# Optimization experiments

Hardware: AMD Instinct MI355X
Metric: run time of the kernel (lower is better)

The kernel has to match this reference:

```python
import jax, jax.numpy as jnp
import numpy as np

DIM = 128
HEADS = 8
DK = DIM // HEADS
HID = DIM * 4
# torch: scores / math.sqrt(scale) with scale = 1/dim**0.5  ->  multiply by dim**0.25
INV = float(1.0 / np.sqrt(1.0 / np.sqrt(DIM)))


def _ln(x, g, b, eps=1e-5):
    m = jnp.mean(x, axis=-1, keepdims=True)
    v = jnp.mean((x - m) ** 2, axis=-1, keepdims=True)
    return (x - m) / jnp.sqrt(v + eps) * g + b


def _lin(x, w, b):  # torch Linear: x @ W.T + b, W:[out,in]
    return jnp.einsum('...i,oi->...o', x, w) + b


def _attention_new(node, edge, w, bv):
    # node [b,n,c], edge [b,n,n,c]; raw torch .view => row-major reshape
    b, n, c = node.shape
    q = _lin(node, w[0], bv[0]).reshape(b, HEADS, n, DK)
    k = _lin(edge, w[1], bv[1]).reshape(b, HEADS, n, n, DK)
    v = _lin(node, w[2], bv[2]).reshape(b, HEADS, n, DK)
    s = jnp.einsum('bhmd,bhmnd->bhmn', q, k) * INV
    out_attn = jax.nn.softmax(s, axis=-1)
    in_attn = jax.nn.softmax(jnp.swapaxes(s, -1, -2), axis=-1)
    eye = jnp.eye(n, dtype=s.dtype)
    # out_attn + in_attn - diag_embed(diagonal(out_attn))
    message = out_attn + in_attn - eye * out_attn
    node_h = jnp.einsum('bhmn,bhnd->bhmd', message, v).reshape(b, n, c)
    edge_h = jnp.einsum('bhmn,bhand->bhamd', message, k).reshape(b, n, n, c)
    return _lin(node_h, w[4], bv[4]), _lin(edge_h, w[3], bv[3]), message


def _enc_dec_attention(mx, px, ma, pa, w, bv):
    b, n, c = mx.shape
    P = px.shape[1]
    qx = _lin(mx, w[0], bv[0]).reshape(b, HEADS, n, DK)
    kx = _lin(px, w[1], bv[1]).reshape(b, HEADS, P, DK)
    vx = _lin(mx, w[2], bv[2]).reshape(b, HEADS, n, DK)
    qa = _lin(ma, w[3], bv[3]).reshape(b, HEADS, n, n, DK)
    ka = _lin(pa, w[4], bv[4]).reshape(b, HEADS, P, P, DK)
    va = _lin(ma, w[5], bv[5]).reshape(b, HEADS, n, n, DK)
    s = jnp.einsum('bhmd,bhnd->bhmn', qx, kx) * INV  # [b,h,n,P]
    out_attn = jax.nn.softmax(s, axis=-1)
    in_attn = jax.nn.softmax(jnp.swapaxes(s, -1, -2), axis=-1)
    message = out_attn + jnp.swapaxes(in_attn, -1, -2)
    # einsum 'bhmn,bhmd->bhmd': sum over n, elementwise scale of v
    node_h = jnp.sum(message, axis=-1)[..., None] * vx
    # 'bhmnd,bhkjd->bhmn': contract d after summing key over (k,j)
    ksum = jnp.sum(ka, axis=(2, 3))  # [b,h,d]
    se = jnp.einsum('bhmnd,bhd->bhmn', qa, ksum) * INV
    oa = jax.nn.softmax(se, axis=-1)
    ia = jax.nn.softmax(jnp.swapaxes(se, -1, -2), axis=-1)
    me = oa + jnp.swapaxes(ia, -1, -2)
    # 'bhmn,bhmkd->bhmnd': contract k
    edge_h = me[..., None] * jnp.sum(va, axis=3)[:, :, :, None, :]
    node_h = _lin(node_h.reshape(b, n, c), w[6], bv[6])
    edge_h = _lin(edge_h.reshape(b, n, n, c), w[7], bv[7])
    return edge_h, node_h, message


def _mlp(x, w1, b1, w2, b2):
    return _lin(jax.nn.sigmoid(_lin(x, w1, b1)), w2, b2)


def _decoder_block(mol_annot, prot_annot, mol_adj, prot_adj,
                   att_w, att_b, dec_w, dec_b,
                   mlp_w1, mlp_b1, mlp_w2, mlp_b2, ln_g, ln_b):
    mx = _ln(mol_annot, ln_g[2], ln_b[2])
    px = _ln(prot_annot, ln_g[3], ln_b[3])
    ma = _ln(mol_adj, ln_g[0], ln_b[0])
    pa = _ln(prot_adj, ln_g[1], ln_b[1])
    px1, pa1, _ = _attention_new(px, pa, att_w, att_b)
    px1 = _ln(px + px1, ln_g[5], ln_b[5])
    pa1 = _ln(pa + pa1, ln_g[4], ln_b[4])
    ma1, mx1, attn_dec = _enc_dec_attention(mx, px1, ma, pa1, dec_w, dec_b)
    ma1 = _ln(ma + ma1, ln_g[6], ln_b[6])
    mx1 = _ln(mx + mx1, ln_g[7], ln_b[7])
    ma2 = _mlp(ma1, mlp_w1[0], mlp_b1[0], mlp_w2[0], mlp_b2[0]) + ma1
    mx2 = _mlp(mx1, mlp_w1[1], mlp_b1[1], mlp_w2[1], mlp_b2[1]) + mx1
    edge_hidden = _ln(ma2, ln_g[8], ln_b[8])
    node_hidden = _ln(mx2, ln_g[9], ln_b[9])
    return edge_hidden, node_hidden, attn_dec


def setup_inputs() -> dict:
    key = jax.random.key(0)
    ks = jax.random.split(key, 16)
    B, N, P = 8, 64, 256
    inp = {
        'mol_annot': jax.random.normal(ks[0], (B, N, DIM), jnp.float32),
        'prot_annot': jax.random.normal(ks[1], (B, P, DIM), jnp.float32),
        'mol_adj': jax.random.normal(ks[2], (B, N, N, DIM), jnp.float32),
        'prot_adj': jax.random.normal(ks[3], (B, P, P, DIM), jnp.float32),
        # Attention_new linears: [q,k,v,out_e,out_n]
        'att_w': jax.random.normal(ks[4], (5, DIM, DIM), jnp.float32) * 0.02,
        'att_b': jax.random.normal(ks[5], (5, DIM), jnp.float32) * 0.02,
        # enc_dec linears: [q_mx,k_px,v_mx,q_ma,k_pa,v_ma,out_mx,out_ma]
        'dec_w': jax.random.normal(ks[6], (8, DIM, DIM), jnp.float32) * 0.02,
        'dec_b': jax.random.normal(ks[7], (8, DIM), jnp.float32) * 0.02,
        # MLPs: index 0 = mlp_ma, 1 = mlp_mx
        'mlp_w1': jax.random.normal(ks[8], (2, HID, DIM), jnp.float32) * 0.02,
        'mlp_b1': jax.random.normal(ks[9], (2, HID), jnp.float32) * 0.02,
        'mlp_w2': jax.random.normal(ks[10], (2, DIM, HID), jnp.float32) * 0.02,
        'mlp_b2': jax.random.normal(ks[11], (2, DIM), jnp.float32) * 0.02,
        # LayerNorms: [ln1_ma,ln1_pa,ln1_mx,ln1_px,ln2_pa,ln2_px,ln3_ma,ln3_mx,ln4_ma,ln4_mx]
        'ln_g': jnp.ones((10, DIM), jnp.float32),
        'ln_b': jnp.zeros((10, DIM), jnp.float32),
    }
    return inp


def reference(mol_annot, prot_annot, mol_adj, prot_adj, att_w, att_b,
              dec_w, dec_b, mlp_w1, mlp_b1, mlp_w2, mlp_b2, ln_g, ln_b):
    return _decoder_block(mol_annot, prot_annot, mol_adj, prot_adj,
                          att_w, att_b, dec_w, dec_b,
                          mlp_w1, mlp_b1, mlp_w2, mlp_b2, ln_g, ln_b)
```

## Files before the change

### kernel.cpp

```cpp
#include <hip/hip_runtime.h>
#include <hip/hip_bf16.h>
#include <math.h>

#define INV_SCALE 3.3635856610148585f

typedef float f32x4 __attribute__((ext_vector_type(4)));
typedef short bf16x8 __attribute__((ext_vector_type(8)));
typedef unsigned short u16;
#define MFMA(a_, b_, c_) __builtin_amdgcn_mfma_f32_16x16x32_bf16(a_, b_, c_, 0, 0, 0)

constexpr int WT_ATT = 0;
constexpr int WT_DEC = 81920;
constexpr int WT_M1  = 212992;
constexpr int WT_M2  = 344064;
constexpr int O_PX   = 475136;
constexpr int O_MX   = 737280;
constexpr int O_MA   = 802816;
constexpr int O_QL   = 4997120;
constexpr int O_VL   = 5259264;
constexpr int O_QXL  = 5521408;
constexpr int O_VXL  = 5586944;
constexpr int O_KXL  = 5652480;
constexpr int O_PX1  = 5914624;
constexpr int O_MX1  = 6176768;
constexpr int O_S    = 6242304;
constexpr int O_MSG  = 10469376;
constexpr int O_NH   = 14663680;
constexpr int O_RS   = 14925824;
constexpr int O_KS   = 14934016;
constexpr int O_SE   = 14935040;
constexpr int O_ME2  = 15197184;
constexpr int O_VAS  = 15459328;
constexpr int O_MROW = 15524864;
constexpr int O_S2   = 15528960;
constexpr int O_MA1  = 16577536;

constexpr int OUT1_OFF = 4194304;
constexpr int OUT2_OFF = 4259840;

__device__ __forceinline__ float waveSum(float v) {
#pragma unroll
  for (int o = 32; o > 0; o >>= 1) v += __shfl_down(v, o, 64);
  return v;
}

__device__ __forceinline__ void split1(float a, u16& h, u16& l) {
  unsigned ua = __float_as_uint(a) & 0xffff0000u;
  h = (u16)(ua >> 16);
  float al = a - __uint_as_float(ua);
  l = (u16)(__float_as_uint(al) >> 16);
}
__device__ __forceinline__ void split8(const float* p, bf16x8& hi, bf16x8& lo) {
#pragma unroll
  for (int i = 0; i < 8; i++) {
    float a = p[i];
    unsigned ua = __float_as_uint(a) & 0xffff0000u;
    float al = a - __uint_as_float(ua);
    hi[i] = (short)(u16)(ua >> 16);
    lo[i] = (short)(u16)(__float_as_uint(al) >> 16);
  }
}
__device__ __forceinline__ u16 rne1(float a) {
  unsigned u = __float_as_uint(a);
  u += 0x7fffu + ((u >> 16) & 1u);
  return (u16)(u >> 16);
}
__device__ __forceinline__ bf16x8 rne8(const float* p) {
  bf16x8 h;
#pragma unroll
  for (int i = 0; i < 8; i++) h[i] = (short)rne1(p[i]);
  return h;
}

__global__ __launch_bounds__(256) void prep_wt(
    const float* __restrict__ att_w, const float* __restrict__ dec_w,
    const float* __restrict__ mlp_w1, const float* __restrict__ mlp_w2,
    float* __restrict__ ws) {
  int seg = blockIdx.x, t = threadIdx.x;
  if (seg < 5) {
    const float* w = att_w + seg * 16384;
    if (seg == 1 || seg == 3) {
      u16* oh = (u16*)(ws + WT_ATT + seg * 16384);
      for (int idx = t; idx < 16384; idx += 256) {
        int e = idx & 7, lane = (idx >> 3) & 63, kk = (idx >> 9) & 3, q = idx >> 11;
        int o = q * 16 + (lane & 15), i = kk * 32 + (lane >> 4) * 8 + e;
        u16 hh, ll; split1(w[o * 128 + i], hh, ll);
        oh[idx] = hh; oh[16384 + idx] = ll;
      }
    } else {
      float* o = ws + WT_ATT + seg * 16384;
      for (int idx = t; idx < 16384; idx += 256) o[idx] = w[(idx & 127) * 128 + (idx >> 7)];
    }
  } else if (seg < 13) {
    int k = seg - 5;
    const float* w = dec_w + k * 16384;
    float* o = ws + WT_DEC + k * 16384;
    for (int idx = t; idx < 16384; idx += 256) o[idx] = w[(idx & 127) * 128 + (idx >> 7)];
  } else if (seg < 15) {
    int k = seg - 13;
    const float* w = mlp_w1 + k * 65536;
    u16* oh = (u16*)(ws + WT_M1 + k * 65536);
    for (int idx = t; idx < 65536; idx += 256) {
      int e = idx & 7, lane = (idx >> 3) & 63, kk = (idx >> 9) & 3, q = idx >> 11;
      int o = q * 16 + (lane & 15), i = kk * 32 + (lane >> 4) * 8 + e;
      oh[idx] = rne1(w[o * 128 + i]); oh[65536 + idx] = 0;
    }
  } else {
    int k = seg - 15;
    const float* w = mlp_w2 + k * 65536;
    u16* oh = (u16*)(ws + WT_M2 + k * 65536);
    for (int idx = t; idx < 65536; idx += 256) {
      int e = idx & 7, lane = (idx >> 3) & 63, kk = (idx >> 9) & 15, q = idx >> 13;
      int o = q * 16 + (lane & 15), i = kk * 32 + (lane >> 4) * 8 + e;
      oh[idx] = rne1(w[o * 512 + i]); oh[65536 + idx] = 0;
    }
  }
}

__global__ __launch_bounds__(128) void ln_rows4(const float* __restrict__ in, float* __restrict__ out,
                                                const float* __restrict__ g, const float* __restrict__ b) {
  int t = threadIdx.x;
  size_t row = (size_t)blockIdx.x * 4 + (t >> 5);
  int c4 = (t & 31) * 4;
  float4 x = *(const float4*)&in[row * 128 + c4];
  float s = x.x + x.y + x.z + x.w;
#pragma unroll
  for (int o = 16; o > 0; o >>= 1) s += __shfl_xor(s, o, 64);
  float mean = s * (1.f / 128.f);
  float dx = x.x - mean, dy = x.y - mean, dz = x.z - mean, dw = x.w - mean;
  float v = dx * dx + dy * dy + dz * dz + dw * dw;
#pragma unroll
  for (int o = 16; o > 0; o >>= 1) v += __shfl_xor(v, o, 64);
  float rstd = rsqrtf(v * (1.f / 128.f) + 1e-5f);
  float4 gv = *(const float4*)&g[c4];
  float4 bv = *(const float4*)&b[c4];
  float4 o4;
  o4.x = dx * rstd * gv.x + bv.x;
  o4.y = dy * rstd * gv.y + bv.y;
  o4.z = dz * rstd * gv.z + bv.z;
  o4.w = dw * rstd * gv.w + bv.w;
  *(float4*)&out[row * 128 + c4] = o4;
}

__global__ __launch_bounds__(128) void lin_rows2(const float* __restrict__ in,
                                                 float* __restrict__ out1, const float* __restrict__ WT1,
                                                 const float* __restrict__ b1v,
                                                 float* __restrict__ out2, const float* __restrict__ WT2,
                                                 const float* __restrict__ b2v) {
  int row = blockIdx.x, t = threadIdx.x;
  __shared__ float rl[128];
  rl[t] = in[(size_t)row * 128 + t];
  __syncthreads();
  float a1 = b1v[t], a2 = b2v[t];
#pragma unroll 8
  for (int i = 0; i < 128; i++) {
    float rv = rl[i];
    a1 += rv * WT1[i * 128 + t];
    a2 += rv * WT2[i * 128 + t];
  }
  out1[(size_t)row * 128 + t] = a1;
  out2[(size_t)row * 128 + t] = a2;
}

__global__ __launch_bounds__(128) void lin_rows(const float* __restrict__ in, float* __restrict__ out,
                                                const float* __restrict__ WT, const float* __restrict__ bias) {
  int row = blockIdx.x, t = threadIdx.x;
  __shared__ float rl[128];
  rl[t] = in[(size_t)row * 128 + t];
  __syncthreads();
  float acc = bias[t];
#pragma unroll 8
  for (int i = 0; i < 128; i++) acc += rl[i] * WT[i * 128 + t];
  out[(size_t)row * 128 + t] = acc;
}

__device__ __forceinline__ void ln32_stats(float (*tile)[132], float* psum, float* meanL, float* rstdL,
                                           int t) {
  int r = t >> 3, seg = t & 7;
  float p = 0;
#pragma unroll
  for (int k = 0; k < 16; k++) p += tile[r][seg * 16 + k];
  psum[r * 8 + seg] = p;
  __syncthreads();
  if (t < 32) { float sm = 0; for (int k = 0; k < 8; k++) sm += psum[t * 8 + k]; meanL[t] = sm * (1.f / 128.f); }
  __syncthreads();
  float mu = meanL[r];
  p = 0;
#pragma unroll
  for (int k = 0; k < 16; k++) { float d = tile[r][seg * 16 + k] - mu; p += d * d; }
  psum[r * 8 + seg] = p;
  __syncthreads();
  if (t < 32) { float sm = 0; for (int k = 0; k < 8; k++) sm += psum[t * 8 + k]; rstdL[t] = rsqrtf(sm * (1.f / 128.f) + 1e-5f); }
  __syncthreads();
}

__device__ __forceinline__ void ln128_stats(float (*tile)[132], float* psum, float* meanL, float* rstdL,
                                            int t) {
  int r = t >> 2, seg = t & 3;
  float p = 0;
#pragma unroll
  for (int k = 0; k < 32; k++) p += tile[r][seg * 32 + k];
  psum[r * 4 + seg] = p;
  __syncthreads();
  if (t < 128) meanL[t] = (psum[t * 4] + psum[t * 4 + 1] + psum[t * 4 + 2] + psum[t * 4 + 3]) * (1.f / 128.f);
  __syncthreads();
  float mu = meanL[r];
  p = 0;
#pragma unroll
  for (int k = 0; k < 32; k++) { float d = tile[r][seg * 32 + k] - mu; p += d * d; }
  psum[r * 4 + seg] = p;
  __syncthreads();
  if (t < 128) rstdL[t] = rsqrtf((psum[t * 4] + psum[t * 4 + 1] + psum[t * 4 + 2] + psum[t * 4 + 3]) * (1.f / 128.f) + 1e-5f);
  __syncthreads();
}

__global__ __launch_bounds__(256, 8) void k1_fold(
    const float* __restrict__ prot_adj, const float* __restrict__ q_lin,
    const float* __restrict__ wk_orig,
    const float* __restrict__ bk,
    const float* __restrict__ g1, const float* __restrict__ b1,
    float* __restrict__ sdst) {
  __shared__ __align__(16) float paF[32][132];
  __shared__ float wq[8][132];
  __shared__ float qL[16];
  __shared__ float psum[256];
  __shared__ float meanL[32], rstdL[32];
  int t = threadIdx.x, bid = blockIdx.x;
  int b = bid >> 11, h = (bid >> 8) & 7, ai = bid & 255;
  int irow = h * 32 + (ai >> 3), j0 = (ai & 7) * 32;
  int mq = (ai >> 3) * 8 + (ai & 7);
  size_t pabase = (((size_t)(b * 256) + irow) * 256 + j0) * 128;
  {
    const float4* src4 = (const float4*)(prot_adj + pabase);
    for (int idx = t; idx < 1024; idx += 256)
      *(float4*)&paF[idx >> 5][(idx & 31) * 4] = src4[idx];
  }
  if (t < 16) qL[t] = q_lin[((size_t)(b * 256) + h * 32 + (mq >> 3)) * 128 + (mq & 7) * 16 + t];
  __syncthreads();
#pragma unroll
  for (int k = 0; k < 4; k++) {
    int o = t + k * 256;
    int g8 = o >> 7, c = o & 127;
    float s = 0;
#pragma unroll
    for (int d = 0; d < 16; d++) s += qL[d] * wk_orig[(g8 * 16 + d) * 128 + c];
    wq[g8][c] = s;
  }
  ln32_stats(paF, psum, meanL, rstdL, t);
  for (int idx = t; idx < 4096; idx += 256) {
    int r = idx >> 7, c = idx & 127;
    paF[r][c] = (paF[r][c] - meanL[r]) * rstdL[r] * g1[c] + b1[c];
  }
  __syncthreads();
  int r = t >> 3, g8 = t & 7;
  float acc = 0;
#pragma unroll
  for (int d = 0; d < 16; d++) acc += qL[d] * bk[g8 * 16 + d];
#pragma unroll 8
  for (int c = 0; c < 128; c++) acc += paF[r][c] * wq[g8][c];
  size_t sb = ((size_t)((b * 8 + h) * 256 + mq)) * 256;
  sdst[sb + t] = INV_SCALE * acc;
}

__global__ __launch_bounds__(256) void col_part(const float* __restrict__ s, float* __restrict__ pmax,
                                                float* __restrict__ psumv) {
  int bid = blockIdx.x, t = threadIdx.x;
  int bh = bid >> 3, ch = bid & 7;
  const float* sp = s + ((size_t)(bh * 256) + ch * 32) * 256 + t;
  float rm = -3.4e38f, rs = 0.f;
  for (int r = 0; r < 32; r++) {
    float x = sp[(size_t)r * 256];
    float nm = fmaxf(rm, x);
    rs = rs * __expf(rm - nm) + __expf(x - nm);
    rm = nm;
  }
  pmax[(bh * 8 + ch) * 256 + t] = rm;
  psumv[(bh * 8 + ch) * 256 + t] = rs;
}

__global__ __launch_bounds__(256, 1) void msg_tiles(const float* __restrict__ s,
                                                    const float* __restrict__ pmax, const float* __restrict__ psumv,
                                                    const float* __restrict__ v_lin,
                                                    u16* __restrict__ mhi, u16* __restrict__ mlo,
                                                    float* __restrict__ nh) {
  __shared__ __align__(16) float rowT[32][260];
  __shared__ float sT[256][33];
  __shared__ __align__(16) u16 vTh[16][264];
  __shared__ __align__(16) u16 vTl[16][264];
  __shared__ float red[256];
  __shared__ float rmax[32], rsinv[32], cmaxL[32], csinvL[32];
  int bid = blockIdx.x, t = threadIdx.x;
  int bh = bid >> 3, m0 = (bid & 7) * 32;
  int b = bh >> 3, h = bh & 7;
  size_t sbase = (size_t)(bh * 256) * 256;
  for (int idx = t; idx < 2048; idx += 256) {
    int r = idx >> 6, c4 = (idx & 63) * 4;
    *(float4*)&rowT[r][c4] = *(const float4*)&s[sbase + (size_t)(m0 + r) * 256 + c4];
  }
  for (int idx = t; idx < 2048; idx += 256) {
    int n = idx >> 3, mc4 = (idx & 7) * 4;
    float4 v4 = *(const float4*)&s[sbase + (size_t)n * 256 + m0 + mc4];
    sT[n][mc4] = v4.x; sT[n][mc4 + 1] = v4.y; sT[n][mc4 + 2] = v4.z; sT[n][mc4 + 3] = v4.w;
  }
  {
    const float4* vb4 = (const float4*)(v_lin + ((size_t)(b * 256) + h * 32) * 128);
    for (int idx = t; idx < 1024; idx += 256) {
      float4 v4 = vb4[idx];
#pragma unroll
      for (int i = 0; i < 4; i++) {
        int flat = idx * 4 + i;
        int d = flat & 15, n = flat >> 4;
        u16 hh2, ll2; split1(((const float*)&v4)[i], hh2, ll2);
        vTh[d][n] = hh2; vTl[d][n] = ll2;
      }
    }
  }
  __syncthreads();
  {
    int r = t >> 3, sg = t & 7;
    float pm = -3.4e38f;
    for (int k = 0; k < 32; k++) pm = fmaxf(pm, rowT[r][sg * 32 + k]);
    red[t] = pm;
    __syncthreads();
    if (t < 32) { float mm = red[t * 8]; for (int k = 1; k < 8; k++) mm = fmaxf(mm, red[t * 8 + k]); rmax[t] = mm; }
    __syncthreads();
    float mm = rmax[r], ps = 0;
    for (int k = 0; k < 32; k++) ps += __expf(rowT[r][sg * 32 + k] - mm);
    red[t] = ps;
    __syncthreads();
    if (t < 32) { float sm = 0; for (int k = 0; k < 8; k++) sm += red[t * 8 + k]; rsinv[t] = 1.f / sm; }
    if (t >= 64 && t < 96) {
      int mc = t - 64, col = m0 + mc;
      float cm = -3.4e38f;
      for (int c2 = 0; c2 < 8; c2++) cm = fmaxf(cm, pmax[(bh * 8 + c2) * 256 + col]);
      float cs = 0;
      for (int c2 = 0; c2 < 8; c2++) cs += psumv[(bh * 8 + c2) * 256 + col] * __expf(pmax[(bh * 8 + c2) * 256 + col] - cm);
      cmaxL[mc] = cm; csinvL[mc] = 1.f / cs;
    }
    __syncthreads();
  }
  for (int idx = t; idx < 8192; idx += 256) {
    int r = idx >> 8, n = idx & 255;
    float x = rowT[r][n];
    float outv = __expf(x - rmax[r]) * rsinv[r];
    float inval = __expf(sT[n][r] - cmaxL[r]) * csinvL[r];
    rowT[r][n] = (n == m0 + r) ? inval : (outv + inval);
  }
  __syncthreads();
  for (int fi = t; fi < 1024; fi += 256) {
    int r = fi >> 5, fc = fi & 31;
    int m = m0 + r;
    int lane = (fc & 3) * 16 + (m & 15);
    size_t base = (size_t)bh * 65536 + (size_t)(m >> 4) * 4096 + (size_t)(fc >> 2) * 512 + lane * 8;
    bf16x8 h8, l8;
    split8(&rowT[r][fc * 8], h8, l8);
    *(bf16x8*)&mhi[base] = h8;
    *(bf16x8*)&mlo[base] = l8;
  }
  int w = t >> 6, l = t & 63, lr = l & 15, lk = l >> 4;
  if (w < 2) {
    f32x4 acc = (f32x4){0.f, 0.f, 0.f, 0.f};
#pragma unroll
    for (int kk = 0; kk < 8; kk++) {
      bf16x8 ah, al;
      split8(&rowT[w * 16 + lr][kk * 32 + lk * 8], ah, al);
      bf16x8 bhv = *(const bf16x8*)&vTh[lr][kk * 32 + lk * 8];
      bf16x8 blv = *(const bf16x8*)&vTl[lr][kk * 32 + lk * 8];
      acc = MFMA(ah, bhv, acc);
      acc = MFMA(al, bhv, acc);
      acc = MFMA(ah, blv, acc);
    }
#pragma unroll
    for (int j = 0; j < 4; j++)
      nh[((size_t)(bh * 256) + m0 + w * 16 + lk * 4 + j) * 16 + lr] = acc[j];
  }
}

__global__ __launch_bounds__(128) void px1_kernel(const float* __restrict__ px, const float* __restrict__ nh,
                                                  const float* __restrict__ WT, const float* __restrict__ bias,
                                                  const float* __restrict__ g, const float* __restrict__ bt,
                                                  float* __restrict__ px1) {
  int p = blockIdx.x, t = threadIdx.x;
  int b = p >> 8, pl = p & 255, h = pl >> 5;
  __shared__ float nodeL[128];
  __shared__ float scr[2];
  nodeL[t] = nh[((size_t)(b * 8 + h) * 256 + ((pl & 31) * 8 + (t >> 4))) * 16 + (t & 15)];
  __syncthreads();
  float acc = bias[t];
#pragma unroll 8
  for (int i = 0; i < 128; i++) acc += nodeL[i] * WT[i * 128 + t];
  float val = px[(size_t)p * 128 + t] + acc;
  float v = waveSum(val);
  if ((t & 63) == 0) scr[t >> 6] = v;
  __syncthreads();
  float mean = (scr[0] + scr[1]) * (1.f / 128.f);
  __syncthreads();
  float dd = val - mean;
  v = waveSum(dd * dd);
  if ((t & 63) == 0) scr[t >> 6] = v;
  __syncthreads();
  float rstd = rsqrtf((scr[0] + scr[1]) * (1.f / 128.f) + 1e-5f);
  px1[(size_t)p * 128 + t] = dd * rstd * g[t] + bt[t];
}

__global__ __launch_bounds__(512, 1) void s2_fused(const float* __restrict__ qxl, const float* __restrict__ kxl,
                                                   float* __restrict__ out2, float* __restrict__ mrow) {
  __shared__ float kxL[256 * 17];
  __shared__ float qxL[64 * 17];
  __shared__ float sL[64][257];
  __shared__ float rmaxL[64], rsinv[64];
  __shared__ float cmaxL[256], csinv[256];
  int bh = blockIdx.x, t = threadIdx.x;
  int b = bh >> 3, h = bh & 7;
  for (int idx = t; idx < 4096; idx += 512) {
    int pl = idx >> 7, cc = idx & 127;
    kxL[(pl * 8 + (cc >> 4)) * 17 + (cc & 15)] = kxl[((size_t)(b * 256) + h * 32 + pl) * 128 + cc];
  }
  for (int idx = t; idx < 1024; idx += 512) {
    int rl = idx >> 7, cc = idx & 127;
    qxL[(rl * 8 + (cc >> 4)) * 17 + (cc & 15)] = qxl[((size_t)(b * 64) + h * 8 + rl) * 128 + cc];
  }
  __syncthreads();
  {
    int p = t & 255, mh = t >> 8;
    float kr[16];
#pragma unroll
    for (int d = 0; d < 16; d++) kr[d] = kxL[p * 17 + d];
    for (int m = mh * 32; m < mh * 32 + 32; m++) {
      float dot = 0;
#pragma unroll
      for (int d = 0; d < 16; d++) dot += qxL[m * 17 + d] * kr[d];
      sL[m][p] = INV_SCALE * dot;
    }
  }
  __syncthreads();
  if (t < 64) {
    float mx = -3.4e38f;
    for (int p = 0; p < 256; p++) mx = fmaxf(mx, sL[t][p]);
    float sm = 0;
    for (int p = 0; p < 256; p++) sm += __expf(sL[t][p] - mx);
    rmaxL[t] = mx; rsinv[t] = 1.f / sm;
  }
  if (t < 256) {
    float mx = -3.4e38f;
    for (int m = 0; m < 64; m++) mx = fmaxf(mx, sL[m][t]);
    float sm = 0;
    for (int m = 0; m < 64; m++) sm += __expf(sL[m][t] - mx);
    cmaxL[t] = mx; csinv[t] = 1.f / sm;
  }
  __syncthreads();
  for (int idx = t; idx < 16384; idx += 512) {
    int m = idx >> 8, p = idx & 255;
    float x = sL[m][p];
    float val = __expf(x - rmaxL[m]) * rsinv[m] + __expf(x - cmaxL[p]) * csinv[p];
    out2[(size_t)bh * 16384 + idx] = val;
    sL[m][p] = val;
  }
  __syncthreads();
  if (t < 64) {
    float sm = 0;
    for (int p = 0; p < 256; p++) sm += sL[t][p];
    mrow[bh * 64 + t] = sm;
  }
}

__global__ __launch_bounds__(128) void mx1_kernel(const float* __restrict__ mx, const float* __restrict__ mrow,
                                                  const float* __restrict__ vxl, const float* __restrict__ WT,
                                                  const float* __restrict__ bias, const float* __restrict__ g,
                                                  const float* __restrict__ bt, float* __restrict__ mx1) {
  int rg = blockIdx.x, t = threadIdx.x;
  int b = rg >> 6, rl = rg & 63, h = rl >> 3;
  __shared__ float nodeL[128];
  __shared__ float scr[2];
  int m = (rl & 7) * 8 + (t >> 4);
  float vxv = vxl[((size_t)(b * 64) + h * 8 + (m >> 3)) * 128 + (m & 7) * 16 + (t & 15)];
  nodeL[t] = mrow[(b * 8 + h) * 64 + m] * vxv;
  __syncthreads();
  float acc = bias[t];
#pragma unroll 8
  for (int i = 0; i < 128; i++) acc += nodeL[i] * WT[i * 128 + t];
  float val = mx[(size_t)rg * 128 + t] + acc;
  float v = waveSum(val);
  if ((t & 63) == 0) scr[t >> 6] = v;
  __syncthreads();
  float mean = (scr[0] + scr[1]) * (1.f / 128.f);
  __syncthreads();
  float dd = val - mean;
  v = waveSum(dd * dd);
  if ((t & 63) == 0) scr[t >> 6] = v;
  __syncthreads();
  float rstd = rsqrtf((scr[0] + scr[1]) * (1.f / 128.f) + 1e-5f);
  mx1[(size_t)rg * 128 + t] = dd * rstd * g[t] + bt[t];
}

__global__ __launch_bounds__(512, 2) void k5_row(
    const float* __restrict__ prot_adj,
    const u16* __restrict__ msg_hi, const u16* __restrict__ msg_lo,
    const u16* __restrict__ wk_hi,
    const u16* __restrict__ wo_hi,
    const float* __restrict__ bk, const float* __restrict__ bo,
    const float* __restrict__ g1, const float* __restrict__ b1,
    const float* __restrict__ g4, const float* __restrict__ b4,
    float* __restrict__ rs128) {
  __shared__ __align__(16) unsigned char Lmem[140800];
  float (*paF)[132] = (float(*)[132])Lmem;
  u16* kBh = (u16*)(Lmem + 67584);
  u16* kBl = (u16*)(Lmem + 67584 + 33792);
  float (*e2)[132] = (float(*)[132])(Lmem + 67584);
  float* psum  = (float*)(Lmem + 135168);
  float* meanL = (float*)(Lmem + 137216);
  float* rstdL = (float*)(Lmem + 137728);
  float* accL  = (float*)(Lmem + 138240);
  float* scr2  = (float*)(Lmem + 138752);
  int t = threadIdx.x;
  int bid = (blockIdx.x & 7) * 256 + (blockIdx.x >> 3);
  int b = bid >> 8, h = (bid >> 5) & 7, irow_rel = bid & 31;
  int irow = h * 32 + irow_rel;
  int w = t >> 6, l = t & 63;
  const int lr = l & 15, lk = l >> 4;
  const size_t mb = ((size_t)(b * 8 + h)) << 16;
  if (t < 128) accL[t] = 0.f;
  for (int half = 0; half < 2; half++) {
    __syncthreads();
    {
      size_t pabase = (((size_t)(b * 256) + irow) * 256 + half * 128) * 128;
      const float4* src4 = (const float4*)(prot_adj + pabase);
      for (int idx = t; idx < 4096; idx += 512)
        *(float4*)&paF[idx >> 5][(idx & 31) * 4] = src4[idx];
    }
    __syncthreads();
    ln128_stats(paF, psum, meanL, rstdL, t);
    for (int idx = t; idx < 16384; idx += 512) {
      int r = idx >> 7, c = idx & 127;
      paF[r][c] = (paF[r][c] - meanL[r]) * rstdL[r] * g1[c] + b1[c];
    }
    __syncthreads();
    {
      f32x4 acc1[8];
#pragma unroll
      for (int q = 0; q < 8; q++) acc1[q] = (f32x4){0.f, 0.f, 0.f, 0.f};
#pragma unroll 1
      for (int kk = 0; kk < 4; kk++) {
        bf16x8 ah, al;
        split8(&paF[w * 16 + lr][kk * 32 + lk * 8], ah, al);
#pragma unroll
        for (int q = 0; q < 8; q++) {
          bf16x8 bh = *(const bf16x8*)&wk_hi[q * 2048 + kk * 512 + l * 8];
          bf16x8 bl = *(const bf16x8*)&wk_hi[16384 + q * 2048 + kk * 512 + l * 8];
          acc1[q] = MFMA(ah, bh, acc1[q]);
          acc1[q] = MFMA(al, bh, acc1[q]);
          acc1[q] = MFMA(ah, bl, acc1[q]);
        }
      }
#pragma unroll
      for (int q = 0; q < 8; q++) {
        float bkv = bk[q * 16 + lr];
#pragma unroll
        for (int j = 0; j < 4; j++) {
          int rloc = w * 16 + lk * 4 + j;
          int n = (rloc & 31) * 8 + q;
          int colB = (rloc >> 5) * 16 + lr;
          u16 hh, ll; split1(acc1[q][j] + bkv, hh, ll);
          kBh[colB * 264 + n] = hh; kBl[colB * 264 + n] = ll;
        }
      }
    }
    __syncthreads();
    f32x4 eacc[2][4];
#pragma unroll
    for (int mt = 0; mt < 2; mt++)
#pragma unroll
      for (int ct = 0; ct < 4; ct++) eacc[mt][ct] = (f32x4){0.f, 0.f, 0.f, 0.f};
#pragma unroll 1
    for (int kk = 0; kk < 8; kk++) {
      bf16x8 bhv[4], blv[4];
#pragma unroll
      for (int ct = 0; ct < 4; ct++) {
        bhv[ct] = *(const bf16x8*)&kBh[(ct * 16 + lr) * 264 + kk * 32 + lk * 8];
        blv[ct] = *(const bf16x8*)&kBl[(ct * 16 + lr) * 264 + kk * 32 + lk * 8];
      }
#pragma unroll
      for (int mt = 0; mt < 2; mt++) {
        size_t ro = mb + (size_t)((w * 2 + mt) * 4096 + kk * 512 + l * 8);
        bf16x8 ah = *(const bf16x8*)&msg_hi[ro];
        bf16x8 al = *(const bf16x8*)&msg_lo[ro];
#pragma unroll
        for (int ct = 0; ct < 4; ct++) {
          eacc[mt][ct] = MFMA(ah, bhv[ct], eacc[mt][ct]);
          eacc[mt][ct] = MFMA(al, bhv[ct], eacc[mt][ct]);
          eacc[mt][ct] = MFMA(ah, blv[ct], eacc[mt][ct]);
        }
      }
    }
    __syncthreads();
#pragma unroll
    for (int mt = 0; mt < 2; mt++)
#pragma unroll
      for (int ct = 0; ct < 4; ct++)
#pragma unroll
        for (int j = 0; j < 4; j++) {
          int m = w * 32 + mt * 16 + lk * 4 + j;
          int colE = ct * 16 + lr;
          e2[(colE >> 4) * 32 + (m >> 3)][(m & 7) * 16 + (colE & 15)] = eacc[mt][ct][j];
        }
    __syncthreads();
    {
      f32x4 oacc[8];
#pragma unroll
      for (int q = 0; q < 8; q++) oacc[q] = (f32x4){0.f, 0.f, 0.f, 0.f};
#pragma unroll 1
      for (int kk = 0; kk < 4; kk++) {
        bf16x8 ah, al;
        split8(&e2[w * 16 + lr][kk * 32 + lk * 8], ah, al);
#pragma unroll
        for (int q = 0; q < 8; q++) {
          bf16x8 bh = *(const bf16x8*)&wo_hi[q * 2048 + kk * 512 + l * 8];
          bf16x8 bl = *(const bf16x8*)&wo_hi[16384 + q * 2048 + kk * 512 + l * 8];
          oacc[q] = MFMA(ah, bh, oacc[q]);
          oacc[q] = MFMA(al, bh, oacc[q]);
          oacc[q] = MFMA(ah, bl, oacc[q]);
        }
      }
      __syncthreads();
#pragma unroll
      for (int q = 0; q < 8; q++) {
        int o = q * 16 + lr;
        float bv = bo[o];
#pragma unroll
        for (int j = 0; j < 4; j++) {
          int rloc = w * 16 + lk * 4 + j;
          paF[rloc][o] = oacc[q][j] + bv + paF[rloc][o];
        }
      }
    }
    __syncthreads();
    ln128_stats(paF, psum, meanL, rstdL, t);
    {
      int c = t & 127, rh = t >> 7;
      float part = 0;
#pragma unroll
      for (int rr = 0; rr < 32; rr++) {
        int r2 = rh * 32 + rr;
        part += (paF[r2][c] - meanL[r2]) * rstdL[r2];
      }
      scr2[rh * 128 + c] = part;
    }
    __syncthreads();
    if (t < 128) accL[t] += scr2[t] + scr2[128 + t] + scr2[256 + t] + scr2[384 + t];
  }
  __syncthreads();
  if (t < 128)
    atomicAdd(&rs128[(b * 8 + h) * 128 + t], g4[t] * accL[t] + 256.f * b4[t]);
}

__global__ __launch_bounds__(128) void ksum_kernel(const float* __restrict__ rs128, const float* __restrict__ WT,
                                                   const float* __restrict__ bias, float* __restrict__ ks) {
  int bh = blockIdx.x, t = threadIdx.x;
  __shared__ float rsL[128];
  __shared__ float pcL[128];
  rsL[t] = rs128[bh * 128 + t];
  __syncthreads();
  float pc = 0;
#pragma unroll 8
  for (int i = 0; i < 128; i++) pc += rsL[i] * WT[i * 128 + t];
  pcL[t] = pc;
  __syncthreads();
  if (t < 16) {
    float kv = 0;
    for (int g8 = 0; g8 < 8; g8++) kv += pcL[g8 * 16 + t] + 8192.f * bias[g8 * 16 + t];
    ks[bh * 16 + t] = kv;
  }
}

__global__ __launch_bounds__(256) void se_vasum(
    const float* __restrict__ ma, const float* __restrict__ WTqa, const float* __restrict__ bqa,
    const float* __restrict__ WTva, const float* __restrict__ bva,
    const float* __restrict__ ks, float* __restrict__ se, float* __restrict__ vas) {
  __shared__ __align__(16) float w[16384];
  __shared__ float rows[16 * 129];
  __shared__ float red[4096];
  int t = threadIdx.x, bid = blockIdx.x;
  int b = bid >> 8, iq = (bid >> 2) & 63, jb = bid & 3, j0 = jb * 16;
  int h = iq >> 3;
  float ksumv[16];
#pragma unroll
  for (int d = 0; d < 16; d++) ksumv[d] = ks[(b * 8 + h) * 16 + d];
  size_t rowbase = ((size_t)(b * 64 + iq) * 64 + j0) * 128;
  for (int idx = t; idx < 2048; idx += 256) rows[(idx >> 7) * 129 + (idx & 127)] = ma[rowbase + idx];
  for (int idx = t; idx < 16384; idx += 256) w[idx] = WTqa[idx];
  __syncthreads();
  int g8 = t >> 5, r = (t >> 1) & 15, iseg = t & 1;
  {
    float acc[16];
#pragma unroll
    for (int d = 0; d < 16; d++) acc[d] = 0.f;
    for (int ii = 0; ii < 64; ii++) {
      int i2 = iseg * 64 + ii;
      float pav = rows[r * 129 + i2];
      float wv[16];
      const float4* w4 = (const float4*)&w[i2 * 128 + g8 * 16];
      *(float4*)&wv[0] = w4[0]; *(float4*)&wv[4] = w4[1]; *(float4*)&wv[8] = w4[2]; *(float4*)&wv[12] = w4[3];
#pragma unroll
      for (int d = 0; d < 16; d++) acc[d] += pav * wv[d];
    }
    float sval = 0;
#pragma unroll
    for (int d = 0; d < 16; d++) sval += acc[d] * ksumv[d];
    red[(r * 8 + g8) * 2 + iseg] = sval;
    __syncthreads();
    if (t < 128) {
      int rr = t >> 3, gg = t & 7;
      float sv = red[(rr * 8 + gg) * 2] + red[(rr * 8 + gg) * 2 + 1];
      float bdot = 0;
#pragma unroll
      for (int d = 0; d < 16; d++) bdot += bqa[gg * 16 + d] * ksumv[d];
      sv += bdot;
      int jj = j0 + rr;
      int mm = (iq & 7) * 8 + (jj >> 3);
      int n2 = (jj & 7) * 8 + gg;
      se[((size_t)(b * 8 + h) * 64 + mm) * 64 + n2] = INV_SCALE * sv;
    }
    __syncthreads();
  }
  for (int idx = t; idx < 16384; idx += 256) w[idx] = WTva[idx];
  __syncthreads();
  {
    float acc[16];
#pragma unroll
    for (int d = 0; d < 16; d++) acc[d] = 0.f;
    for (int ii = 0; ii < 64; ii++) {
      int i2 = iseg * 64 + ii;
      float pav = rows[r * 129 + i2];
      float wv[16];
      const float4* w4 = (const float4*)&w[i2 * 128 + g8 * 16];
      *(float4*)&wv[0] = w4[0]; *(float4*)&wv[4] = w4[1]; *(float4*)&wv[8] = w4[2]; *(float4*)&wv[12] = w4[3];
#pragma unroll
      for (int d = 0; d < 16; d++) acc[d] += pav * wv[d];
    }
    if (iseg == 0) {
#pragma unroll
      for (int d = 0; d < 16; d++) acc[d] += bva[g8 * 16 + d];
    }
#pragma unroll
    for (int d = 0; d < 16; d++) red[t * 16 + d] = acc[d];
    __syncthreads();
    if (t < 32) {
      int mgrp = t >> 4, d = t & 15;
      float sm = 0;
      for (int gg = 0; gg < 8; gg++)
        for (int rr = mgrp * 8; rr < mgrp * 8 + 8; rr++) {
          sm += red[(gg * 32 + rr * 2) * 16 + d] + red[(gg * 32 + rr * 2 + 1) * 16 + d];
        }
      int mv = (iq & 7) * 8 + jb * 2 + mgrp;
      atomicAdd(&vas[((size_t)(b * 8 + h) * 64 + mv) * 16 + d], sm);
    }
  }
}

__global__ __launch_bounds__(256) void me2_kernel(const float* __restrict__ se, float* __restrict__ me2) {
  __shared__ float sL[64 * 65];
  __shared__ float rmaxL[64], rsinv[64], cmaxL[64], csinv[64];
  int bh = blockIdx.x, t = threadIdx.x;
  for (int idx = t; idx < 4096; idx += 256) sL[(idx >> 6) * 65 + (idx & 63)] = se[(size_t)bh * 4096 + idx];
  __syncthreads();
  if (t < 64) {
    float mx = -3.4e38f;
    for (int n = 0; n < 64; n++) mx = fmaxf(mx, sL[t * 65 + n]);
    float sm = 0;
    for (int n = 0; n < 64; n++) sm += __expf(sL[t * 65 + n] - mx);
    rmaxL[t] = mx; rsinv[t] = 1.f / sm;
  } else if (t < 128) {
    int n = t - 64;
    float mx = -3.4e38f;
    for (int m = 0; m < 64; m++) mx = fmaxf(mx, sL[m * 65 + n]);
    float sm = 0;
    for (int m = 0; m < 64; m++) sm += __expf(sL[m * 65 + n] - mx);
    cmaxL[n] = mx; csinv[n] = 1.f / sm;
  }
  __syncthreads();
  for (int idx = t; idx < 4096; idx += 256) {
    int m = idx >> 6, n = idx & 63;
    float x = sL[m * 65 + n];
    me2[(size_t)bh * 4096 + idx] = __expf(x - rmaxL[m]) * rsinv[m] + __expf(x - cmaxL[n]) * csinv[n];
  }
}

__global__ __launch_bounds__(256) void ma1_kernel(
    const float* __restrict__ ma, const float* __restrict__ me2, const float* __restrict__ vas,
    const float* __restrict__ WT, const float* __restrict__ bias,
    const float* __restrict__ g, const float* __restrict__ bt, float* __restrict__ ma1) {
  __shared__ __align__(16) float w[16384];
  __shared__ float rows[16 * 129];
  __shared__ float ored[4096];
  __shared__ float psum[256];
  __shared__ float meanL[16], rstdL[16];
  int t = threadIdx.x, bid = blockIdx.x;
  int b = bid >> 8, iq = (bid >> 2) & 63, jb = bid & 3, j0 = jb * 16;
  int h = iq >> 3;
  int bh64 = (b * 8 + h) * 64;
  size_t rowbase = ((size_t)(b * 64 + iq) * 64 + j0) * 128;
  for (int idx = t; idx < 2048; idx += 256) {
    int r = idx >> 7, c = idx & 127;
    int mm = (iq & 7) * 8 + jb * 2 + (r >> 3);
    int nn = (r & 7) * 8 + (c >> 4);
    rows[r * 129 + c] = me2[(size_t)(bh64 + mm) * 64 + nn] * vas[(size_t)(bh64 + mm) * 16 + (c & 15)];
  }
  for (int idx = t; idx < 16384; idx += 256) w[idx] = WT[idx];
  __syncthreads();
  int g8 = t >> 5, r = (t >> 1) & 15, iseg = t & 1;
  {
    float acc[16];
#pragma unroll
    for (int d = 0; d < 16; d++) acc[d] = 0.f;
    for (int ii = 0; ii < 64; ii++) {
      int i2 = iseg * 64 + ii;
      float pav = rows[r * 129 + i2];
      float wv[16];
      const float4* w4 = (const float4*)&w[i2 * 128 + g8 * 16];
      *(float4*)&wv[0] = w4[0]; *(float4*)&wv[4] = w4[1]; *(float4*)&wv[8] = w4[2]; *(float4*)&wv[12] = w4[3];
#pragma unroll
      for (int d = 0; d < 16; d++) acc[d] += pav * wv[d];
    }
    float* od = &ored[(iseg * 16 + r) * 128 + g8 * 16];
#pragma unroll
    for (int d = 0; d < 16; d++) od[d] = acc[d];
  }
  __syncthreads();
  for (int idx = t; idx < 2048; idx += 256) {
    int r2 = idx >> 7, c = idx & 127;
    rows[r2 * 129 + c] = ored[r2 * 128 + c] + ored[(16 + r2) * 128 + c] + bias[c] + ma[rowbase + idx];
  }
  __syncthreads();
  {
    int rr = t >> 4, seg = t & 15;
    float p = 0;
#pragma unroll
    for (int k = 0; k < 8; k++) p += rows[rr * 129 + seg * 8 + k];
    psum[rr * 16 + seg] = p;
    __syncthreads();
    if (t < 16) { float sm = 0; for (int k = 0; k < 16; k++) sm += psum[t * 16 + k]; meanL[t] = sm * (1.f / 128.f); }
    __syncthreads();
    float mu = meanL[rr];
    p = 0;
#pragma unroll
    for (int k = 0; k < 8; k++) { float d = rows[rr * 129 + seg * 8 + k] - mu; p += d * d; }
    psum[rr * 16 + seg] = p;
    __syncthreads();
    if (t < 16) { float sm = 0; for (int k = 0; k < 16; k++) sm += psum[t * 16 + k]; rstdL[t] = rsqrtf(sm * (1.f / 128.f) + 1e-5f); }
    __syncthreads();
  }
  for (int idx = t; idx < 2048; idx += 256) {
    int r2 = idx >> 7, c = idx & 127;
    ma1[rowbase + idx] = (rows[r2 * 129 + c] - meanL[r2]) * rstdL[r2] * g[c] + bt[c];
  }
}

__global__ __launch_bounds__(256, 4) void mlp_mfma(
    const float* __restrict__ in,
    const u16* __restrict__ w1h,
    const float* __restrict__ b1,
    const u16* __restrict__ w2h,
    const float* __restrict__ b2,
    const float* __restrict__ g, const float* __restrict__ bt, float* __restrict__ out) {
  __shared__ __align__(16) float rowL[16][132];
  __shared__ __align__(16) u16 hh[16][520];
  __shared__ float psum[256];
  __shared__ float meanL[16], rstdL[16];
  int t = threadIdx.x, bid = blockIdx.x;
  int w = t >> 6, l = t & 63, lr = l & 15, lk = l >> 4;
  size_t base = (size_t)bid * 2048;
  {
    const float4* src4 = (const float4*)(in + base);
    for (int idx = t; idx < 512; idx += 256)
      *(float4*)&rowL[idx >> 5][(idx & 31) * 4] = src4[idx];
  }
  __syncthreads();
  {
    f32x4 acc1[8];
#pragma unroll
    for (int nt = 0; nt < 8; nt++) acc1[nt] = (f32x4){0.f, 0.f, 0.f, 0.f};
#pragma unroll 1
    for (int kk = 0; kk < 4; kk++) {
      bf16x8 ah = rne8(&rowL[lr][kk * 32 + lk * 8]);
#pragma unroll
      for (int nt = 0; nt < 8; nt++) {
        int q = w * 8 + nt;
        bf16x8 bh = *(const bf16x8*)&w1h[q * 2048 + kk * 512 + l * 8];
        acc1[nt] = MFMA(ah, bh, acc1[nt]);
      }
    }
#pragma unroll
    for (int nt = 0; nt < 8; nt++) {
      int o = w * 128 + nt * 16 + lr;
      float bb = b1[o];
#pragma unroll
      for (int j = 0; j < 4; j++) {
        int m = lk * 4 + j;
        float hv = 1.f / (1.f + __expf(-(acc1[nt][j] + bb)));
        hh[m][o] = rne1(hv);
      }
    }
  }
  __syncthreads();
  {
    f32x4 acc2[2];
#pragma unroll
    for (int nt = 0; nt < 2; nt++) acc2[nt] = (f32x4){0.f, 0.f, 0.f, 0.f};
#pragma unroll 1
    for (int kk = 0; kk < 16; kk++) {
      bf16x8 ah = *(const bf16x8*)&hh[lr][kk * 32 + lk * 8];
#pragma unroll
      for (int nt = 0; nt < 2; nt++) {
        int q = w * 2 + nt;
        bf16x8 bh = *(const bf16x8*)&w2h[q * 8192 + kk * 512 + l * 8];
        acc2[nt] = MFMA(ah, bh, acc2[nt]);
      }
    }
    __syncthreads();
#pragma unroll
    for (int nt = 0; nt < 2; nt++) {
      int c = w * 32 + nt * 16 + lr;
      float bb = b2[c];
#pragma unroll
      for (int j = 0; j < 4; j++) {
        int m = lk * 4 + j;
        rowL[m][c] = acc2[nt][j] + bb + rowL[m][c];
      }
    }
  }
  __syncthreads();
  {
    int rr = t >> 4, seg = t & 15;
    float p = 0;
#pragma unroll
    for (int k = 0; k < 8; k++) p += rowL[rr][seg * 8 + k];
    psum[rr * 16 + seg] = p;
    __syncthreads();
    if (t < 16) { float sm = 0; for (int k = 0; k < 16; k++) sm += psum[t * 16 + k]; meanL[t] = sm * (1.f / 128.f); }
    __syncthreads();
    float mu = meanL[rr];
    p = 0;
#pragma unroll
    for (int k = 0; k < 8; k++) { float d = rowL[rr][seg * 8 + k] - mu; p += d * d; }
    psum[rr * 16 + seg] = p;
    __syncthreads();
    if (t < 16) { float sm = 0; for (int k = 0; k < 16; k++) sm += psum[t * 16 + k]; rstdL[t] = rsqrtf(sm * (1.f / 128.f) + 1e-5f); }
    __syncthreads();
  }
  for (int idx = t; idx < 2048; idx += 256) {
    int r2 = idx >> 7, cc = idx & 127;
    out[base + idx] = (rowL[r2][cc] - meanL[r2]) * rstdL[r2] * g[cc] + bt[cc];
  }
}

extern "C" void kernel_launch(void* const* d_in, const int* in_sizes, int n_in,
                              void* d_out, int out_size, void* d_ws, size_t ws_size,
                              hipStream_t stream) {
  (void)in_sizes; (void)n_in; (void)out_size; (void)ws_size;
  const float* mol_annot  = (const float*)d_in[0];
  const float* prot_annot = (const float*)d_in[1];
  const float* mol_adj    = (const float*)d_in[2];
  const float* prot_adj   = (const float*)d_in[3];
  const float* att_w = (const float*)d_in[4];
  const float* att_b = (const float*)d_in[5];
  const float* dec_w = (const float*)d_in[6];
  const float* dec_b = (const float*)d_in[7];
  const float* mlp_w1 = (const float*)d_in[8];
  const float* mlp_b1 = (const float*)d_in[9];
  const float* mlp_w2 = (const float*)d_in[10];
  const float* mlp_b2 = (const float*)d_in[11];
  const float* ln_g = (const float*)d_in[12];
  const float* ln_b = (const float*)d_in[13];
  float* out = (float*)d_out;
  float* ws = (float*)d_ws;

  const u16* wk_hi = (const u16*)(ws + WT_ATT + 16384);
  const u16* wo_hi = (const u16*)(ws + WT_ATT + 3 * 16384);
  u16* msg_hi = (u16*)(ws + O_MA1);
  u16* msg_lo = msg_hi + 4194304;
  float* pmaxp = ws + O_MSG;
  float* psump = ws + O_MSG + 131072;

  hipMemsetAsync(ws + O_RS, 0, 8192 * sizeof(float), stream);
  hipMemsetAsync(ws + O_VAS, 0, 65536 * sizeof(float), stream);
  prep_wt<<<17, 256, 0, stream>>>(att_w, dec_w, mlp_w1, mlp_w2, ws);
  ln_rows4<<<512, 128, 0, stream>>>(prot_annot, ws + O_PX, ln_g + 384, ln_b + 384);
  ln_rows4<<<128, 128, 0, stream>>>(mol_annot, ws + O_MX, ln_g + 256, ln_b + 256);
  ln_rows4<<<8192, 128, 0, stream>>>(mol_adj, ws + O_MA, ln_g, ln_b);
  lin_rows2<<<2048, 128, 0, stream>>>(ws + O_PX, ws + O_QL, ws + WT_ATT, att_b,
                                      ws + O_VL, ws + WT_ATT + 2 * 16384, att_b + 256);
  lin_rows2<<<512, 128, 0, stream>>>(ws + O_MX, ws + O_QXL, ws + WT_DEC, dec_b,
                                     ws + O_VXL, ws + WT_DEC + 2 * 16384, dec_b + 256);
  k1_fold<<<16384, 256, 0, stream>>>(prot_adj, ws + O_QL, att_w + 16384, att_b + 128,
                                     ln_g + 128, ln_b + 128, ws + O_S);
  col_part<<<512, 256, 0, stream>>>(ws + O_S, pmaxp, psump);
  msg_tiles<<<512, 256, 0, stream>>>(ws + O_S, pmaxp, psump, ws + O_VL, msg_hi, msg_lo, ws + O_NH);
  px1_kernel<<<2048, 128, 0, stream>>>(ws + O_PX, ws + O_NH, ws + WT_ATT + 4 * 16384, att_b + 512,
                                       ln_g + 640, ln_b + 640, ws + O_PX1);
  lin_rows<<<2048, 128, 0, stream>>>(ws + O_PX1, ws + O_KXL, ws + WT_DEC + 16384, dec_b + 128);
  s2_fused<<<64, 512, 0, stream>>>(ws + O_QXL, ws + O_KXL, out + OUT2_OFF, ws + O_MROW);
  mx1_kernel<<<512, 128, 0, stream>>>(ws + O_MX, ws + O_MROW, ws + O_VXL, ws + WT_DEC + 6 * 16384,
                                      dec_b + 768, ln_g + 896, ln_b + 896, ws + O_MX1);
  k5_row<<<2048, 512, 0, stream>>>(prot_adj, msg_hi, msg_lo, wk_hi, wo_hi,
                                   att_b + 128, att_b + 384,
                                   ln_g + 128, ln_b + 128, ln_g + 512, ln_b + 512, ws + O_RS);
  ksum_kernel<<<64, 128, 0, stream>>>(ws + O_RS, ws + WT_DEC + 4 * 16384, dec_b + 512, ws + O_KS);
  se_vasum<<<2048, 256, 0, stream>>>(ws + O_MA, ws + WT_DEC + 3 * 16384, dec_b + 384,
                                     ws + WT_DEC + 5 * 16384, dec_b + 640, ws + O_KS, ws + O_SE, ws + O_VAS);
  me2_kernel<<<64, 256, 0, stream>>>(ws + O_SE, ws + O_ME2);
  ma1_kernel<<<2048, 256, 0, stream>>>(ws + O_MA, ws + O_ME2, ws + O_VAS, ws + WT_DEC + 7 * 16384,
                                       dec_b + 896, ln_g + 768, ln_b + 768, ws + O_MA1);
  mlp_mfma<<<2048, 256, 0, stream>>>(ws + O_MA1, (const u16*)(ws + WT_M1), mlp_b1,
                                     (const u16*)(ws + WT_M2), mlp_b2,
                                     ln_g + 1024, ln_b + 1024, out);
  mlp_mfma<<<32, 256, 0, stream>>>(ws + O_MX1, (const u16*)(ws + WT_M1 + 65536), mlp_b1 + 512,
                                   (const u16*)(ws + WT_M2 + 65536), mlp_b2 + 128,
                                   ln_g + 1152, ln_b + 1152, out + OUT1_OFF);
}
```

Measured before the change: 891.4 us.

## Process k5_row in 64-row chunks to halve LDS and double occupancy

The k5_row kernel now walks each row's 256 columns in four 64-row chunks instead of two 128-row halves. This roughly halves the shared-memory footprint, and the launch bounds are raised to allow 4 blocks per CU. The 8 waves are split into 4 row groups × 2 output-column groups for the K and O projections, and each wave keeps fewer accumulators. The goal is more resident waves to hide latency, at the cost of more loop iterations, more barriers, and reloading the weights once per chunk.

```diff
diff --git a/kernel.cpp b/kernel.cpp
--- a/kernel.cpp
+++ b/kernel.cpp
@@ -194,23 +194,23 @@
   __syncthreads();
 }
 
-__device__ __forceinline__ void ln128_stats(float (*tile)[132], float* psum, float* meanL, float* rstdL,
-                                            int t) {
-  int r = t >> 2, seg = t & 3;
+__device__ __forceinline__ void ln64_stats(float (*tile)[132], float* psum, float* meanL, float* rstdL,
+                                           int t) {
+  int r = t >> 3, seg = t & 7;
   float p = 0;
 #pragma unroll
-  for (int k = 0; k < 32; k++) p += tile[r][seg * 32 + k];
-  psum[r * 4 + seg] = p;
-  __syncthreads();
-  if (t < 128) meanL[t] = (psum[t * 4] + psum[t * 4 + 1] + psum[t * 4 + 2] + psum[t * 4 + 3]) * (1.f / 128.f);
+  for (int k = 0; k < 16; k++) p += tile[r][seg * 16 + k];
+  psum[r * 8 + seg] = p;
+  __syncthreads();
+  if (t < 64) { float sm = 0; for (int k = 0; k < 8; k++) sm += psum[t * 8 + k]; meanL[t] = sm * (1.f / 128.f); }
   __syncthreads();
   float mu = meanL[r];
   p = 0;
 #pragma unroll
-  for (int k = 0; k < 32; k++) { float d = tile[r][seg * 32 + k] - mu; p += d * d; }
-  psum[r * 4 + seg] = p;
-  __syncthreads();
-  if (t < 128) rstdL[t] = rsqrtf((psum[t * 4] + psum[t * 4 + 1] + psum[t * 4 + 2] + psum[t * 4 + 3]) * (1.f / 128.f) + 1e-5f);
+  for (int k = 0; k < 16; k++) { float d = tile[r][seg * 16 + k] - mu; p += d * d; }
+  psum[r * 8 + seg] = p;
+  __syncthreads();
+  if (t < 64) { float sm = 0; for (int k = 0; k < 8; k++) sm += psum[t * 8 + k]; rstdL[t] = rsqrtf(sm * (1.f / 128.f) + 1e-5f); }
   __syncthreads();
 }
 
@@ -493,7 +493,7 @@
   mx1[(size_t)rg * 128 + t] = dd * rstd * g[t] + bt[t];
 }
 
-__global__ __launch_bounds__(512, 2) void k5_row(
+__global__ __launch_bounds__(512, 4) void k5_row(
     const float* __restrict__ prot_adj,
     const u16* __restrict__ msg_hi, const u16* __restrict__ msg_lo,
     const u16* __restrict__ wk_hi,
@@ -502,80 +502,83 @@
     const float* __restrict__ g1, const float* __restrict__ b1,
     const float* __restrict__ g4, const float* __restrict__ b4,
     float* __restrict__ rs128) {
-  __shared__ __align__(16) unsigned char Lmem[140800];
+  __shared__ __align__(16) unsigned char Lmem[72704];
   float (*paF)[132] = (float(*)[132])Lmem;
-  u16* kBh = (u16*)(Lmem + 67584);
-  u16* kBl = (u16*)(Lmem + 67584 + 33792);
-  float (*e2)[132] = (float(*)[132])(Lmem + 67584);
-  float* psum  = (float*)(Lmem + 135168);
-  float* meanL = (float*)(Lmem + 137216);
-  float* rstdL = (float*)(Lmem + 137728);
-  float* accL  = (float*)(Lmem + 138240);
-  float* scr2  = (float*)(Lmem + 138752);
+  u16* kBh = (u16*)(Lmem + 33792);
+  u16* kBl = (u16*)(Lmem + 33792 + 16896);
+  float (*e2)[132] = (float(*)[132])(Lmem + 33792);
+  float* psum  = (float*)(Lmem + 67584);
+  float* meanL = (float*)(Lmem + 69632);
+  float* rstdL = (float*)(Lmem + 69888);
+  float* accL  = (float*)(Lmem + 70144);
+  float* scr2  = (float*)(Lmem + 70656);
   int t = threadIdx.x;
   int bid = (blockIdx.x & 7) * 256 + (blockIdx.x >> 3);
   int b = bid >> 8, h = (bid >> 5) & 7, irow_rel = bid & 31;
   int irow = h * 32 + irow_rel;
   int w = t >> 6, l = t & 63;
   const int lr = l & 15, lk = l >> 4;
+  const int wr = w & 3, wq = w >> 2;
   const size_t mb = ((size_t)(b * 8 + h)) << 16;
   if (t < 128) accL[t] = 0.f;
-  for (int half = 0; half < 2; half++) {
+  for (int chunk = 0; chunk < 4; chunk++) {
     __syncthreads();
     {
-      size_t pabase = (((size_t)(b * 256) + irow) * 256 + half * 128) * 128;
+      size_t pabase = (((size_t)(b * 256) + irow) * 256 + chunk * 64) * 128;
       const float4* src4 = (const float4*)(prot_adj + pabase);
-      for (int idx = t; idx < 4096; idx += 512)
+      for (int idx = t; idx < 2048; idx += 512)
         *(float4*)&paF[idx >> 5][(idx & 31) * 4] = src4[idx];
     }
     __syncthreads();
-    ln128_stats(paF, psum, meanL, rstdL, t);
-    for (int idx = t; idx < 16384; idx += 512) {
+    ln64_stats(paF, psum, meanL, rstdL, t);
+    for (int idx = t; idx < 8192; idx += 512) {
       int r = idx >> 7, c = idx & 127;
       paF[r][c] = (paF[r][c] - meanL[r]) * rstdL[r] * g1[c] + b1[c];
     }
     __syncthreads();
     {
-      f32x4 acc1[8];
-#pragma unroll
-      for (int q = 0; q < 8; q++) acc1[q] = (f32x4){0.f, 0.f, 0.f, 0.f};
+      f32x4 acc1[4];
+#pragma unroll
+      for (int qq = 0; qq < 4; qq++) acc1[qq] = (f32x4){0.f, 0.f, 0.f, 0.f};
 #pragma unroll 1
       for (int kk = 0; kk < 4; kk++) {
         bf16x8 ah, al;
-        split8(&paF[w * 16 + lr][kk * 32 + lk * 8], ah, al);
-#pragma unroll
-        for (int q = 0; q < 8; q++) {
+        split8(&paF[wr * 16 + lr][kk * 32 + lk * 8], ah, al);
+#pragma unroll
+        for (int qq = 0; qq < 4; qq++) {
+          int q = wq * 4 + qq;
           bf16x8 bh = *(const bf16x8*)&wk_hi[q * 2048 + kk * 512 + l * 8];
           bf16x8 bl = *(const bf16x8*)&wk_hi[16384 + q * 2048 + kk * 512 + l * 8];
-          acc1[q] = MFMA(ah, bh, acc1[q]);
-          acc1[q] = MFMA(al, bh, acc1[q]);
-          acc1[q] = MFMA(ah, bl, acc1[q]);
+          acc1[qq] = MFMA(ah, bh, acc1[qq]);
+          acc1[qq] = MFMA(al, bh, acc1[qq]);
+          acc1[qq] = MFMA(ah, bl, acc1[qq]);
         }
       }
 #pragma unroll
-      for (int q = 0; q < 8; q++) {
+      for (int qq = 0; qq < 4; qq++) {
+        int q = wq * 4 + qq;
         float bkv = bk[q * 16 + lr];
 #pragma unroll
         for (int j = 0; j < 4; j++) {
-          int rloc = w * 16 + lk * 4 + j;
+          int rloc = wr * 16 + lk * 4 + j;
           int n = (rloc & 31) * 8 + q;
           int colB = (rloc >> 5) * 16 + lr;
-          u16 hh, ll; split1(acc1[q][j] + bkv, hh, ll);
+          u16 hh, ll; split1(acc1[qq][j] + bkv, hh, ll);
           kBh[colB * 264 + n] = hh; kBl[colB * 264 + n] = ll;
         }
       }
     }
     __syncthreads();
-    f32x4 eacc[2][4];
+    f32x4 eacc[2][2];
 #pragma unroll
     for (int mt = 0; mt < 2; mt++)
 #pragma unroll
-      for (int ct = 0; ct < 4; ct++) eacc[mt][ct] = (f32x4){0.f, 0.f, 0.f, 0.f};
+      for (int ct = 0; ct < 2; ct++) eacc[mt][ct] = (f32x4){0.f, 0.f, 0.f, 0.f};
 #pragma unroll 1
     for (int kk = 0; kk < 8; kk++) {
-      bf16x8 bhv[4], blv[4];
-#pragma unroll
-      for (int ct = 0; ct < 4; ct++) {
+      bf16x8 bhv[2], blv[2];
+#pragma unroll
+      for (int ct = 0; ct < 2; ct++) {
         bhv[ct] = *(const bf16x8*)&kBh[(ct * 16 + lr) * 264 + kk * 32 + lk * 8];
         blv[ct] = *(const bf16x8*)&kBl[(ct * 16 + lr) * 264 + kk * 32 + lk * 8];
       }
@@ -585,7 +588,7 @@
         bf16x8 ah = *(const bf16x8*)&msg_hi[ro];
         bf16x8 al = *(const bf16x8*)&msg_lo[ro];
 #pragma unroll
-        for (int ct = 0; ct < 4; ct++) {
+        for (int ct = 0; ct < 2; ct++) {
           eacc[mt][ct] = MFMA(ah, bhv[ct], eacc[mt][ct]);
           eacc[mt][ct] = MFMA(al, bhv[ct], eacc[mt][ct]);
           eacc[mt][ct] = MFMA(ah, blv[ct], eacc[mt][ct]);
@@ -596,7 +599,7 @@
 #pragma unroll
     for (int mt = 0; mt < 2; mt++)
 #pragma unroll
-      for (int ct = 0; ct < 4; ct++)
+      for (int ct = 0; ct < 2; ct++)
 #pragma unroll
         for (int j = 0; j < 4; j++) {
           int m = w * 32 + mt * 16 + lk * 4 + j;
@@ -605,42 +608,43 @@
         }
     __syncthreads();
     {
-      f32x4 oacc[8];
-#pragma unroll
-      for (int q = 0; q < 8; q++) oacc[q] = (f32x4){0.f, 0.f, 0.f, 0.f};
+      f32x4 oacc[4];
+#pragma unroll
+      for (int qq = 0; qq < 4; qq++) oacc[qq] = (f32x4){0.f, 0.f, 0.f, 0.f};
 #pragma unroll 1
       for (int kk = 0; kk < 4; kk++) {
         bf16x8 ah, al;
-        split8(&e2[w * 16 + lr][kk * 32 + lk * 8], ah, al);
-#pragma unroll
-        for (int q = 0; q < 8; q++) {
+        split8(&e2[wr * 16 + lr][kk * 32 + lk * 8], ah, al);
+#pragma unroll
+        for (int qq = 0; qq < 4; qq++) {
+          int q = wq * 4 + qq;
           bf16x8 bh = *(const bf16x8*)&wo_hi[q * 2048 + kk * 512 + l * 8];
           bf16x8 bl = *(const bf16x8*)&wo_hi[16384 + q * 2048 + kk * 512 + l * 8];
-          oacc[q] = MFMA(ah, bh, oacc[q]);
-          oacc[q] = MFMA(al, bh, oacc[q]);
-          oacc[q] = MFMA(ah, bl, oacc[q]);
+          oacc[qq] = MFMA(ah, bh, oacc[qq]);
+          oacc[qq] = MFMA(al, bh, oacc[qq]);
+          oacc[qq] = MFMA(ah, bl, oacc[qq]);
         }
       }
       __syncthreads();
 #pragma unroll
-      for (int q = 0; q < 8; q++) {
-        int o = q * 16 + lr;
+      for (int qq = 0; qq < 4; qq++) {
+        int o = (wq * 4 + qq) * 16 + lr;
         float bv = bo[o];
 #pragma unroll
         for (int j = 0; j < 4; j++) {
-          int rloc = w * 16 + lk * 4 + j;
-          paF[rloc][o] = oacc[q][j] + bv + paF[rloc][o];
+          int rloc = wr * 16 + lk * 4 + j;
+          paF[rloc][o] = oacc[qq][j] + bv + paF[rloc][o];
         }
       }
     }
     __syncthreads();
-    ln128_stats(paF, psum, meanL, rstdL, t);
+    ln64_stats(paF, psum, meanL, rstdL, t);
     {
       int c = t & 127, rh = t >> 7;
       float part = 0;
 #pragma unroll
-      for (int rr = 0; rr < 32; rr++) {
-        int r2 = rh * 32 + rr;
+      for (int rr = 0; rr < 16; rr++) {
+        int r2 = rh * 16 + rr;
         part += (paF[r2][c] - meanL[r2]) * rstdL[r2];
       }
       scr2[rh * 128 + c] = part;
```

After: 841.6 us. 5.6% less time.
